# Optimization experiments

Hardware: AMD Instinct MI355X
Metric: run time of the kernel (lower is better)

The kernel has to match this reference:

```python
import jax, jax.numpy as jnp
import numpy as np
from jax import lax

N_EXPERTS = 8


def setup_inputs() -> dict:
    key = jax.random.key(0)
    ks = jax.random.split(key, 5)
    B, F, H, C, E = 32768, 512, 256, 100, N_EXPERTS
    x = jax.random.normal(ks[0], (B, F), dtype=jnp.float32)
    W1 = jax.random.normal(ks[1], (E, F, H), dtype=jnp.float32) * (1.0 / np.sqrt(F))
    b1 = jnp.zeros((E, H), dtype=jnp.float32)
    W2 = jax.random.normal(ks[2], (E, H, C), dtype=jnp.float32) * (1.0 / np.sqrt(H))
    b2 = jnp.zeros((E, C), dtype=jnp.float32)
    Wg = jax.random.normal(ks[3], (F, E), dtype=jnp.float32) * (1.0 / np.sqrt(F))
    return {"x": x, "W1": W1, "b1": b1, "W2": W2, "b2": b2, "Wg": Wg, "k": 2}


def reference(x, W1, b1, W2, b2, Wg, k):
    B = x.shape[0]
    # experts: per-expert 2-layer MLP, vectorized over the expert dim e
    h = jax.nn.relu(jnp.einsum('bf,efh->ebh', x, W1) + b1[:, None, :])  # [E,B,H]
    preds = jnp.einsum('ebh,ehc->ebc', h, W2) + b2[:, None, :]          # [E,B,C]
    # fixed gating: softmax over gate logits, top-k, hard 1/k weights
    probs = jax.nn.softmax(x @ Wg, axis=-1)                             # [B,E]
    _, top_idx = lax.top_k(probs, k)                                    # [B,k]
    weights = jnp.zeros_like(probs).at[jnp.arange(B)[:, None], top_idx].set(1.0 / k)
    # combined prediction: gate-weighted sum of per-expert softmaxed logits
    combined = jnp.einsum('ebc,be->bc', jax.nn.softmax(preds, axis=-1), weights)
    part_sizes = (weights > 0).sum(axis=0)  # samples routed per expert
    return combined, preds, part_sizes
```

## Files before the change

kernel.cpp:

```cpp
#include <hip/hip_runtime.h>
#include <hip/hip_bf16.h>
#include <math.h>

#define B_ 32768
#define F_ 512
#define H_ 256
#define C_ 100
#define CP 112
#define E_ 8

typedef __attribute__((ext_vector_type(8))) short bf16x8;
typedef __attribute__((ext_vector_type(4))) float f32x4;

__device__ __forceinline__ unsigned short f2b(float f) {
    unsigned int u = __float_as_uint(f);
    return (unsigned short)((u + 0x7fffu + ((u >> 16) & 1u)) >> 16);
}

__device__ __forceinline__ void gll16(const void* g, void* l) {
    __builtin_amdgcn_global_load_lds((__attribute__((address_space(1))) void*)(g),
                                     (__attribute__((address_space(3))) void*)(l),
                                     16, 0, 0);
}

__global__ __launch_bounds__(256) void k0_cvt_x(const float* __restrict__ x,
                                                unsigned short* __restrict__ xb) {
    size_t t = (size_t)blockIdx.x * 256 + threadIdx.x;
    #pragma unroll
    for (int it = 0; it < 4; ++it) {
        size_t i4 = t + (size_t)it * (4096 * 256);
        float4 v = ((const float4*)x)[i4];
        ushort4 o;
        o.x = f2b(v.x); o.y = f2b(v.y); o.z = f2b(v.z); o.w = f2b(v.w);
        ((ushort4*)xb)[i4] = o;
    }
}

__global__ __launch_bounds__(256) void k0_tr_w1(const float* __restrict__ W1,
                                                unsigned short* __restrict__ w1t) {
    __shared__ float tile[32][33];
    int e = blockIdx.z, fb = blockIdx.x * 32, hb = blockIdx.y * 32;
    int tx = threadIdx.x, ty = threadIdx.y;
    #pragma unroll
    for (int j = 0; j < 4; ++j)
        tile[ty + 8 * j][tx] = W1[((size_t)(e * F_ + fb + ty + 8 * j)) * H_ + hb + tx];
    __syncthreads();
    #pragma unroll
    for (int j = 0; j < 4; ++j)
        w1t[((size_t)(e * H_ + hb + ty + 8 * j)) * F_ + fb + tx] = f2b(tile[tx][ty + 8 * j]);
}

__global__ __launch_bounds__(256) void k0_cvt_w2(const float* __restrict__ W2,
                                                 unsigned short* __restrict__ w2t) {
    int idx = blockIdx.x * 256 + threadIdx.x;
    if (idx >= E_ * CP * H_) return;
    int e = idx / (CP * H_);
    int r = idx - e * (CP * H_);
    int c = r / H_, h = r - c * H_;
    float v = (c < C_) ? W2[((size_t)(e * H_ + h)) * C_ + c] : 0.0f;
    w2t[idx] = f2b(v);
}

__global__ __launch_bounds__(256) void k1_gate(const float* __restrict__ x,
                                               const float* __restrict__ Wg,
                                               int* __restrict__ routes,
                                               float* __restrict__ part) {
    __shared__ float sWg[F_ * E_];
    __shared__ int cnt[E_];
    int tid = threadIdx.x;
    for (int i = tid; i < F_ * E_; i += 256) sWg[i] = Wg[i];
    if (tid < E_) cnt[tid] = 0;
    __syncthreads();

    int r = tid >> 3, eidx = tid & 7;
    int row = blockIdx.x * 32 + r;
    const float* xr = x + (size_t)row * F_;
    double acc = 0.0;
    for (int f = 0; f < F_; f += 4) {
        float4 xv = *(const float4*)(xr + f);
        acc += (double)xv.x * (double)sWg[(f + 0) * 8 + eidx];
        acc += (double)xv.y * (double)sWg[(f + 1) * 8 + eidx];
        acc += (double)xv.z * (double)sWg[(f + 2) * 8 + eidx];
        acc += (double)xv.w * (double)sWg[(f + 3) * 8 + eidx];
    }
    double v = acc; int ie = eidx;
    #pragma unroll
    for (int off = 1; off < 8; off <<= 1) {
        double ov = __shfl_xor(v, off);
        int oi = __shfl_xor(ie, off);
        if (ov > v || (ov == v && oi < ie)) { v = ov; ie = oi; }
    }
    int e1 = ie;
    double v2 = (eidx == e1) ? -1e300 : acc; int ie2 = eidx;
    #pragma unroll
    for (int off = 1; off < 8; off <<= 1) {
        double ov = __shfl_xor(v2, off);
        int oi = __shfl_xor(ie2, off);
        if (ov > v2 || (ov == v2 && oi < ie2)) { v2 = ov; ie2 = oi; }
    }
    int e2 = ie2;
    if (eidx == 0) {
        routes[row] = e1 | (e2 << 3);
        atomicAdd(&cnt[e1], 1);
        atomicAdd(&cnt[e2], 1);
    }
    __syncthreads();
    if (tid < E_) atomicAdd(&part[tid], (float)cnt[tid]);
}

__global__ __launch_bounds__(256) void k2_moe(const unsigned short* __restrict__ xbf,
                                              const unsigned short* __restrict__ w1t,
                                              const unsigned short* __restrict__ w2t,
                                              const float* __restrict__ b1,
                                              const float* __restrict__ b2,
                                              float* __restrict__ preds) {
    __shared__ __align__(16) char smem[40960];
    const int tid = threadIdx.x;
    const int w = tid >> 6, lane = tid & 63;
    const int q = lane >> 4, ln = lane & 15;
    const int e = blockIdx.y;
    const int rowBase = blockIdx.x * 64;

    const int sub = lane >> 3;
    const int j8 = (lane & 7) ^ sub;
    const unsigned short* srcA0 = xbf + (size_t)(rowBase + w * 8 + sub) * F_ + 8 * j8;
    const unsigned short* srcB0 = w1t + (size_t)(e * H_ + w * 8 + sub) * F_ + 8 * j8;
    char* dstA = smem + w * 1024;
    char* dstB = smem + 8192 + w * 1024;

    float bias1[4];
    #pragma unroll
    for (int nt = 0; nt < 4; ++nt) bias1[nt] = b1[e * H_ + w * 64 + nt * 16 + ln];

    f32x4 acc[4][4];
    #pragma unroll
    for (int i = 0; i < 4; ++i)
        #pragma unroll
        for (int j = 0; j < 4; ++j) acc[i][j] = (f32x4){0.f, 0.f, 0.f, 0.f};

    for (int kk = 0; kk < 8; ++kk) {
        const int ko = kk * 64;
        gll16(srcA0 + ko, dstA);
        gll16(srcA0 + 32 * F_ + ko, dstA + 4096);
        #pragma unroll
        for (int i = 0; i < 8; ++i)
            gll16(srcB0 + (size_t)i * 32 * F_ + ko, dstB + i * 4096);
        __syncthreads();
        #pragma unroll
        for (int ks = 0; ks < 2; ++ks) {
            const int slot = ((ks * 4 + q) ^ (ln & 7)) * 16;
            bf16x8 af[4], bfr[4];
            #pragma unroll
            for (int mt = 0; mt < 4; ++mt)
                af[mt] = *(const bf16x8*)(smem + (mt * 16 + ln) * 128 + slot);
            #pragma unroll
            for (int nt = 0; nt < 4; ++nt)
                bfr[nt] = *(const bf16x8*)(smem + 8192 + (w * 64 + nt * 16 + ln) * 128 + slot);
            #pragma unroll
            for (int mt = 0; mt < 4; ++mt)
                #pragma unroll
                for (int nt = 0; nt < 4; ++nt)
                    acc[mt][nt] = __builtin_amdgcn_mfma_f32_16x16x32_bf16(af[mt], bfr[nt], acc[mt][nt], 0, 0, 0);
        }
        __syncthreads();
    }

    #pragma unroll
    for (int mt = 0; mt < 4; ++mt)
        #pragma unroll
        for (int nt = 0; nt < 4; ++nt)
            #pragma unroll
            for (int r2 = 0; r2 < 4; ++r2) {
                int rr = mt * 16 + q * 4 + r2;
                int col = w * 64 + nt * 16 + ln;
                float v = fmaxf(acc[mt][nt][r2] + bias1[nt], 0.0f);
                *(unsigned short*)(smem + rr * 528 + col * 2) = f2b(v);
            }

    const unsigned short* w2base = w2t + ((size_t)e * CP + ln) * H_ + q * 8;
    bf16x8 wreg[2][7];
    #pragma unroll
    for (int mt = 0; mt < 7; ++mt)
        wreg[0][mt] = *(const bf16x8*)(w2base + mt * 16 * H_);

    f32x4 acc2[7];
    #pragma unroll
    for (int i = 0; i < 7; ++i) acc2[i] = (f32x4){0.f, 0.f, 0.f, 0.f};
    const int offH = (w * 16 + ln) * 528 + q * 16;

    __syncthreads();

    #pragma unroll
    for (int kc = 0; kc < 8; ++kc) {
        const int cur = kc & 1, nxt = cur ^ 1;
        if (kc < 7) {
            #pragma unroll
            for (int mt = 0; mt < 7; ++mt)
                wreg[nxt][mt] = *(const bf16x8*)(w2base + mt * 16 * H_ + (kc + 1) * 32);
        }
        bf16x8 hb = *(const bf16x8*)(smem + offH + kc * 64);
        #pragma unroll
        for (int mt = 0; mt < 7; ++mt)
            acc2[mt] = __builtin_amdgcn_mfma_f32_16x16x32_bf16(wreg[cur][mt], hb, acc2[mt], 0, 0, 0);
    }

    int row = rowBase + w * 16 + ln;
    #pragma unroll
    for (int mt = 0; mt < 7; ++mt) {
        int c0 = mt * 16 + q * 4;
        if (c0 + 3 < C_) {
            f32x4 bias = *(const f32x4*)(b2 + e * C_ + c0);
            f32x4 o = acc2[mt] + bias;
            *(f32x4*)(preds + ((size_t)e * B_ + row) * C_ + c0) = o;
        }
    }
}

__global__ __launch_bounds__(256) void k3_combine(const float* __restrict__ preds,
                                                  const int* __restrict__ routes,
                                                  float* __restrict__ combined) {
    __shared__ float pbuf[4][104];
    int tid = threadIdx.x, wv = tid >> 6, lane = tid & 63;
    int row = blockIdx.x * 2 + (wv >> 1);
    int rt = routes[row];
    int e = (wv & 1) ? ((rt >> 3) & 7) : (rt & 7);
    const float* pr = preds + ((size_t)e * B_ + row) * C_;
    float a0 = (lane < C_) ? pr[lane] : -1e30f;
    float a1 = (lane + 64 < C_) ? pr[lane + 64] : -1e30f;
    float m = fmaxf(a0, a1);
    #pragma unroll
    for (int off = 32; off; off >>= 1) m = fmaxf(m, __shfl_xor(m, off));
    float s0 = (lane < C_) ? expf(a0 - m) : 0.f;
    float s1 = (lane + 64 < C_) ? expf(a1 - m) : 0.f;
    float s = s0 + s1;
    #pragma unroll
    for (int off = 32; off; off >>= 1) s += __shfl_xor(s, off);
    float inv = 0.5f / s;
    if (lane < C_) pbuf[wv][lane] = s0 * inv;
    if (lane + 64 < C_) pbuf[wv][lane + 64] = s1 * inv;
    __syncthreads();
    if (tid < C_)
        combined[(size_t)(blockIdx.x * 2) * C_ + tid] = pbuf[0][tid] + pbuf[1][tid];
    else if (tid >= 128 && tid < 128 + C_)
        combined[(size_t)(blockIdx.x * 2 + 1) * C_ + (tid - 128)] = pbuf[2][tid - 128] + pbuf[3][tid - 128];
}

extern "C" void kernel_launch(void* const* d_in, const int* in_sizes, int n_in,
                              void* d_out, int out_size, void* d_ws, size_t ws_size,
                              hipStream_t stream) {
    (void)in_sizes; (void)n_in; (void)out_size;
    const float* x  = (const float*)d_in[0];
    const float* W1 = (const float*)d_in[1];
    const float* b1 = (const float*)d_in[2];
    const float* W2 = (const float*)d_in[3];
    const float* b2 = (const float*)d_in[4];
    const float* Wg = (const float*)d_in[5];

    float* out = (float*)d_out;
    float* combined = out;
    float* preds = out + (size_t)B_ * C_;
    float* part  = out + (size_t)B_ * C_ + (size_t)E_ * B_ * C_;

    char* ws = (char*)d_ws;
    unsigned short* xbf = (unsigned short*)ws;
    unsigned short* w1t = (unsigned short*)(ws + 33554432);
    unsigned short* w2t = (unsigned short*)(ws + 35651584);
    int* routes = (int*)(ws + 36110336);
    if (ws_size < 36241408) return;

    hipMemsetAsync(part, 0, E_ * sizeof(float), stream);
    k0_cvt_x<<<4096, 256, 0, stream>>>(x, xbf);
    k0_tr_w1<<<dim3(F_ / 32, H_ / 32, E_), dim3(32, 8), 0, stream>>>(W1, w1t);
    k0_cvt_w2<<<(E_ * CP * H_ + 255) / 256, 256, 0, stream>>>(W2, w2t);
    k1_gate<<<B_ / 32, 256, 0, stream>>>(x, Wg, routes, part);
    k2_moe<<<dim3(B_ / 64, E_), 256, 0, stream>>>(xbf, w1t, w2t, b1, b2, preds);
    k3_combine<<<B_ / 2, 256, 0, stream>>>(preds, routes, combined);
}
```

Before: 421.4 us.

## Fuse gate with x conversion and shrink MoE K-tile for higher occupancy

Merges the bf16 conversion of x with the gating matmul and top-2 selection, so x is read from global memory once instead of twice. Each row is now handled by 32 threads that reduce 8 double-precision accumulators with shuffles. The expert GEMM kernel halves its K-step (32 instead of 64) and swaps the A/B operand roles, cutting shared memory to 32KB and requesting 5 blocks per CU. The hidden-layer staging now uses an XOR-swizzled layout, and the double-buffered W2 register prefetch is replaced by a single buffer. The trade-off is twice as many barrier-synchronised K iterations and less latency hiding on the W2 loads.

```diff
diff --git a/kernel.cpp b/kernel.cpp
--- a/kernel.cpp
+++ b/kernel.cpp
@@ -23,17 +23,64 @@
                                      16, 0, 0);
 }
 
-__global__ __launch_bounds__(256) void k0_cvt_x(const float* __restrict__ x,
-                                                unsigned short* __restrict__ xb) {
-    size_t t = (size_t)blockIdx.x * 256 + threadIdx.x;
+__global__ __launch_bounds__(256) void k0_gate(const float* __restrict__ x,
+                                               const float* __restrict__ Wg,
+                                               unsigned short* __restrict__ xb,
+                                               int* __restrict__ routes,
+                                               float* __restrict__ part) {
+    __shared__ float sWgT[E_ * F_];
+    __shared__ int cnt[E_];
+    const int tid = threadIdx.x;
+    for (int i = tid; i < E_ * F_; i += 256) {
+        int e = i & 7, f = i >> 3;
+        sWgT[e * F_ + f] = Wg[i];
+    }
+    if (tid < E_) cnt[tid] = 0;
+    __syncthreads();
+
+    const int r = tid >> 5, c = tid & 31;
+    const int row = blockIdx.x * 8 + r;
+    const float* xr = x + (size_t)row * F_;
+    double acc8[8];
+    #pragma unroll
+    for (int e = 0; e < 8; ++e) acc8[e] = 0.0;
+
     #pragma unroll
     for (int it = 0; it < 4; ++it) {
-        size_t i4 = t + (size_t)it * (4096 * 256);
-        float4 v = ((const float4*)x)[i4];
+        int f0 = it * 128 + c * 4;
+        float4 xv = *(const float4*)(xr + f0);
         ushort4 o;
-        o.x = f2b(v.x); o.y = f2b(v.y); o.z = f2b(v.z); o.w = f2b(v.w);
-        ((ushort4*)xb)[i4] = o;
-    }
+        o.x = f2b(xv.x); o.y = f2b(xv.y); o.z = f2b(xv.z); o.w = f2b(xv.w);
+        *(ushort4*)(xb + (size_t)row * F_ + f0) = o;
+        #pragma unroll
+        for (int e = 0; e < 8; ++e) {
+            f32x4 wv = *(const f32x4*)(sWgT + e * F_ + f0);
+            acc8[e] += (double)xv.x * (double)wv[0];
+            acc8[e] += (double)xv.y * (double)wv[1];
+            acc8[e] += (double)xv.z * (double)wv[2];
+            acc8[e] += (double)xv.w * (double)wv[3];
+        }
+    }
+    #pragma unroll
+    for (int off = 16; off; off >>= 1)
+        #pragma unroll
+        for (int e = 0; e < 8; ++e) acc8[e] += __shfl_xor(acc8[e], off);
+
+    if (c == 0) {
+        double best = -1e300, second = -1e300;
+        int e1 = 0, e2 = 0;
+        #pragma unroll
+        for (int e = 0; e < 8; ++e) {
+            double v = acc8[e];
+            if (v > best) { second = best; e2 = e1; best = v; e1 = e; }
+            else if (v > second) { second = v; e2 = e; }
+        }
+        routes[row] = e1 | (e2 << 3);
+        atomicAdd(&cnt[e1], 1);
+        atomicAdd(&cnt[e2], 1);
+    }
+    __syncthreads();
+    if (tid < E_) atomicAdd(&part[tid], (float)cnt[tid]);
 }
 
 __global__ __launch_bounds__(256) void k0_tr_w1(const float* __restrict__ W1,
@@ -61,76 +108,30 @@
     w2t[idx] = f2b(v);
 }
 
-__global__ __launch_bounds__(256) void k1_gate(const float* __restrict__ x,
-                                               const float* __restrict__ Wg,
-                                               int* __restrict__ routes,
-                                               float* __restrict__ part) {
-    __shared__ float sWg[F_ * E_];
-    __shared__ int cnt[E_];
-    int tid = threadIdx.x;
-    for (int i = tid; i < F_ * E_; i += 256) sWg[i] = Wg[i];
-    if (tid < E_) cnt[tid] = 0;
-    __syncthreads();
-
-    int r = tid >> 3, eidx = tid & 7;
-    int row = blockIdx.x * 32 + r;
-    const float* xr = x + (size_t)row * F_;
-    double acc = 0.0;
-    for (int f = 0; f < F_; f += 4) {
-        float4 xv = *(const float4*)(xr + f);
-        acc += (double)xv.x * (double)sWg[(f + 0) * 8 + eidx];
-        acc += (double)xv.y * (double)sWg[(f + 1) * 8 + eidx];
-        acc += (double)xv.z * (double)sWg[(f + 2) * 8 + eidx];
-        acc += (double)xv.w * (double)sWg[(f + 3) * 8 + eidx];
-    }
-    double v = acc; int ie = eidx;
-    #pragma unroll
-    for (int off = 1; off < 8; off <<= 1) {
-        double ov = __shfl_xor(v, off);
-        int oi = __shfl_xor(ie, off);
-        if (ov > v || (ov == v && oi < ie)) { v = ov; ie = oi; }
-    }
-    int e1 = ie;
-    double v2 = (eidx == e1) ? -1e300 : acc; int ie2 = eidx;
-    #pragma unroll
-    for (int off = 1; off < 8; off <<= 1) {
-        double ov = __shfl_xor(v2, off);
-        int oi = __shfl_xor(ie2, off);
-        if (ov > v2 || (ov == v2 && oi < ie2)) { v2 = ov; ie2 = oi; }
-    }
-    int e2 = ie2;
-    if (eidx == 0) {
-        routes[row] = e1 | (e2 << 3);
-        atomicAdd(&cnt[e1], 1);
-        atomicAdd(&cnt[e2], 1);
-    }
-    __syncthreads();
-    if (tid < E_) atomicAdd(&part[tid], (float)cnt[tid]);
-}
-
-__global__ __launch_bounds__(256) void k2_moe(const unsigned short* __restrict__ xbf,
-                                              const unsigned short* __restrict__ w1t,
-                                              const unsigned short* __restrict__ w2t,
-                                              const float* __restrict__ b1,
-                                              const float* __restrict__ b2,
-                                              float* __restrict__ preds) {
-    __shared__ __align__(16) char smem[40960];
+__global__ __launch_bounds__(256, 5) void k2_moe(const unsigned short* __restrict__ xbf,
+                                                 const unsigned short* __restrict__ w1t,
+                                                 const unsigned short* __restrict__ w2t,
+                                                 const float* __restrict__ b1,
+                                                 const float* __restrict__ b2,
+                                                 float* __restrict__ preds) {
+    __shared__ __align__(16) char smem[32768];
     const int tid = threadIdx.x;
     const int w = tid >> 6, lane = tid & 63;
     const int q = lane >> 4, ln = lane & 15;
     const int e = blockIdx.y;
     const int rowBase = blockIdx.x * 64;
 
-    const int sub = lane >> 3;
-    const int j8 = (lane & 7) ^ sub;
-    const unsigned short* srcA0 = xbf + (size_t)(rowBase + w * 8 + sub) * F_ + 8 * j8;
-    const unsigned short* srcB0 = w1t + (size_t)(e * H_ + w * 8 + sub) * F_ + 8 * j8;
+    const int sub = lane >> 2;
+    const int j4 = (lane & 3) ^ (sub & 3);
+    const unsigned short* srcA = xbf + (size_t)(rowBase + w * 16 + sub) * F_ + 8 * j4;
+    const unsigned short* srcB = w1t + (size_t)(e * H_ + w * 16 + sub) * F_ + 8 * j4;
     char* dstA = smem + w * 1024;
-    char* dstB = smem + 8192 + w * 1024;
-
-    float bias1[4];
-    #pragma unroll
-    for (int nt = 0; nt < 4; ++nt) bias1[nt] = b1[e * H_ + w * 64 + nt * 16 + ln];
+    char* dstB = smem + 4096 + w * 1024;
+
+    f32x4 bias1v[4];
+    #pragma unroll
+    for (int mt = 0; mt < 4; ++mt)
+        bias1v[mt] = *(const f32x4*)(b1 + e * H_ + w * 64 + mt * 16 + q * 4);
 
     f32x4 acc[4][4];
     #pragma unroll
@@ -138,70 +139,71 @@
         #pragma unroll
         for (int j = 0; j < 4; ++j) acc[i][j] = (f32x4){0.f, 0.f, 0.f, 0.f};
 
-    for (int kk = 0; kk < 8; ++kk) {
-        const int ko = kk * 64;
-        gll16(srcA0 + ko, dstA);
-        gll16(srcA0 + 32 * F_ + ko, dstA + 4096);
-        #pragma unroll
-        for (int i = 0; i < 8; ++i)
-            gll16(srcB0 + (size_t)i * 32 * F_ + ko, dstB + i * 4096);
+    const int fsl = (q ^ (ln & 3)) * 16;
+    for (int kk = 0; kk < 16; ++kk) {
+        const int ko = kk * 32;
+        gll16(srcA + ko, dstA);
+        #pragma unroll
+        for (int i = 0; i < 4; ++i)
+            gll16(srcB + (size_t)i * 64 * F_ + ko, dstB + i * 4096);
         __syncthreads();
-        #pragma unroll
-        for (int ks = 0; ks < 2; ++ks) {
-            const int slot = ((ks * 4 + q) ^ (ln & 7)) * 16;
-            bf16x8 af[4], bfr[4];
-            #pragma unroll
-            for (int mt = 0; mt < 4; ++mt)
-                af[mt] = *(const bf16x8*)(smem + (mt * 16 + ln) * 128 + slot);
+        bf16x8 af[4], bfr[4];
+        #pragma unroll
+        for (int mt = 0; mt < 4; ++mt)
+            af[mt] = *(const bf16x8*)(smem + 4096 + (w * 64 + mt * 16 + ln) * 64 + fsl);
+        #pragma unroll
+        for (int nt = 0; nt < 4; ++nt)
+            bfr[nt] = *(const bf16x8*)(smem + (nt * 16 + ln) * 64 + fsl);
+        #pragma unroll
+        for (int mt = 0; mt < 4; ++mt)
             #pragma unroll
             for (int nt = 0; nt < 4; ++nt)
-                bfr[nt] = *(const bf16x8*)(smem + 8192 + (w * 64 + nt * 16 + ln) * 128 + slot);
-            #pragma unroll
-            for (int mt = 0; mt < 4; ++mt)
-                #pragma unroll
-                for (int nt = 0; nt < 4; ++nt)
-                    acc[mt][nt] = __builtin_amdgcn_mfma_f32_16x16x32_bf16(af[mt], bfr[nt], acc[mt][nt], 0, 0, 0);
-        }
+                acc[mt][nt] = __builtin_amdgcn_mfma_f32_16x16x32_bf16(af[mt], bfr[nt], acc[mt][nt], 0, 0, 0);
         __syncthreads();
     }
 
     #pragma unroll
-    for (int mt = 0; mt < 4; ++mt)
-        #pragma unroll
-        for (int nt = 0; nt < 4; ++nt)
-            #pragma unroll
-            for (int r2 = 0; r2 < 4; ++r2) {
-                int rr = mt * 16 + q * 4 + r2;
-                int col = w * 64 + nt * 16 + ln;
-                float v = fmaxf(acc[mt][nt][r2] + bias1[nt], 0.0f);
-                *(unsigned short*)(smem + rr * 528 + col * 2) = f2b(v);
-            }
+    for (int mt = 0; mt < 4; ++mt) {
+        const int ch = w * 8 + mt * 2 + (q >> 1);
+        const int inner = (q & 1) * 8;
+        #pragma unroll
+        for (int nt = 0; nt < 4; ++nt) {
+            const int xrow = nt * 16 + ln;
+            float v0 = fmaxf(acc[mt][nt][0] + bias1v[mt][0], 0.0f);
+            float v1 = fmaxf(acc[mt][nt][1] + bias1v[mt][1], 0.0f);
+            float v2 = fmaxf(acc[mt][nt][2] + bias1v[mt][2], 0.0f);
+            float v3 = fmaxf(acc[mt][nt][3] + bias1v[mt][3], 0.0f);
+            uint2 pv;
+            pv.x = (unsigned)f2b(v0) | ((unsigned)f2b(v1) << 16);
+            pv.y = (unsigned)f2b(v2) | ((unsigned)f2b(v3) << 16);
+            *(uint2*)(smem + xrow * 512 + ((ch ^ (xrow & 7)) * 16) + inner) = pv;
+        }
+    }
 
     const unsigned short* w2base = w2t + ((size_t)e * CP + ln) * H_ + q * 8;
-    bf16x8 wreg[2][7];
+    bf16x8 wreg[7];
     #pragma unroll
     for (int mt = 0; mt < 7; ++mt)
-        wreg[0][mt] = *(const bf16x8*)(w2base + mt * 16 * H_);
+        wreg[mt] = *(const bf16x8*)(w2base + mt * 16 * H_);
 
     f32x4 acc2[7];
     #pragma unroll
     for (int i = 0; i < 7; ++i) acc2[i] = (f32x4){0.f, 0.f, 0.f, 0.f};
-    const int offH = (w * 16 + ln) * 528 + q * 16;
+    const int hrow = w * 16 + ln;
 
     __syncthreads();
 
     #pragma unroll
     for (int kc = 0; kc < 8; ++kc) {
-        const int cur = kc & 1, nxt = cur ^ 1;
+        bf16x8 hb = *(const bf16x8*)(smem + hrow * 512 + (((kc * 4 + q) ^ (hrow & 7)) * 16));
+        #pragma unroll
+        for (int mt = 0; mt < 7; ++mt)
+            acc2[mt] = __builtin_amdgcn_mfma_f32_16x16x32_bf16(wreg[mt], hb, acc2[mt], 0, 0, 0);
         if (kc < 7) {
             #pragma unroll
             for (int mt = 0; mt < 7; ++mt)
-                wreg[nxt][mt] = *(const bf16x8*)(w2base + mt * 16 * H_ + (kc + 1) * 32);
-        }
-        bf16x8 hb = *(const bf16x8*)(smem + offH + kc * 64);
-        #pragma unroll
-        for (int mt = 0; mt < 7; ++mt)
-            acc2[mt] = __builtin_amdgcn_mfma_f32_16x16x32_bf16(wreg[cur][mt], hb, acc2[mt], 0, 0, 0);
+                wreg[mt] = *(const bf16x8*)(w2base + mt * 16 * H_ + (kc + 1) * 32);
+        }
     }
 
     int row = rowBase + w * 16 + ln;
@@ -269,10 +271,9 @@
     if (ws_size < 36241408) return;
 
     hipMemsetAsync(part, 0, E_ * sizeof(float), stream);
-    k0_cvt_x<<<4096, 256, 0, stream>>>(x, xbf);
+    k0_gate<<<B_ / 8, 256, 0, stream>>>(x, Wg, xbf, routes, part);
     k0_tr_w1<<<dim3(F_ / 32, H_ / 32, E_), dim3(32, 8), 0, stream>>>(W1, w1t);
     k0_cvt_w2<<<(E_ * CP * H_ + 255) / 256, 256, 0, stream>>>(W2, w2t);
-    k1_gate<<<B_ / 32, 256, 0, stream>>>(x, Wg, routes, part);
     k2_moe<<<dim3(B_ / 64, E_), 256, 0, stream>>>(xbf, w1t, w2t, b1, b2, preds);
     k3_combine<<<B_ / 2, 256, 0, stream>>>(preds, routes, combined);
 }
```

New measurement: 448.8 us. +6.5%, slower.
